# Kernel optimization log

Measured on AMD Instinct MI355X. Metric: run time of the kernel, lower is better.

The kernel has to match this reference:

```python
import jax, jax.numpy as jnp
import numpy as np

CH = (16, 32, 16)
T_STEPS = 30
THRESH = 1.0


def conv3d(x, w, b):
    # x: (B, Cin, D, H, W), w: (Cout, Cin, kD, kH, kW), stride 2, VALID
    y = jax.lax.conv_general_dilated(
        x, w, window_strides=(2, 2, 2), padding='VALID',
        dimension_numbers=('NCDHW', 'OIDHW', 'NCDHW'))
    return y + b[None, :, None, None, None]


def setup_inputs() -> dict:
    key = jax.random.key(0)
    ks = jax.random.split(key, 11)
    B = 4
    x = jax.random.normal(ks[0], (B, 24, 602, 602), jnp.float32)

    def uinit(k, shape, fan_in):
        bound = 1.0 / np.sqrt(fan_in)
        return jax.random.uniform(k, shape, jnp.float32, -bound, bound)

    fan1 = 1 * 3 * 15 * 15
    fan2 = CH[0] * 3 * 15 * 15
    fan3 = CH[1] * 3 * 15 * 15
    w1 = uinit(ks[1], (CH[0], 1, 3, 15, 15), fan1)
    b1 = uinit(ks[2], (CH[0],), fan1)
    w2 = uinit(ks[3], (CH[1], CH[0], 3, 15, 15), fan2)
    b2 = uinit(ks[4], (CH[1],), fan2)
    w3 = uinit(ks[5], (CH[2], CH[1], 3, 15, 15), fan3)
    b3 = uinit(ks[6], (CH[2],), fan3)
    F1 = 21632 * CH[2] // 16  # 21632 for CH[2]=16
    fc1_w = uinit(ks[7], (512, F1), F1)
    fc1_b = uinit(ks[8], (512,), F1)
    fc2_w = uinit(ks[9], (54, 512), 512)
    fc2_b = uinit(ks[10], (54,), 512)
    return dict(x=x, w1=w1, b1=b1, w2=w2, b2=b2, w3=w3, b3=b3,
                fc1_w=fc1_w, fc1_b=fc1_b, fc2_w=fc2_w, fc2_b=fc2_b)


def _forward(x, w1, b1, w2, b2, w3, b3, fc1_w, fc1_b, fc2_w, fc2_b):
    B = x.shape[0]
    # avg_pool2d(kernel=2): (B,24,602,602) -> (B,24,301,301)
    xp = x.reshape(B, 24, 301, 2, 301, 2).mean(axis=(3, 5))
    h = xp[:, None]  # (B,1,24,301,301)
    h = jax.nn.relu(conv3d(h, w1, b1))  # (B,16,11,144,144)
    h = jax.nn.relu(conv3d(h, w2, b2))  # (B,32,5,65,65)
    h = jax.nn.relu(conv3d(h, w3, b3))  # (B,16,2,26,26)
    x_snn = h.reshape(B, -1)            # (B, 21632)

    sgn = jnp.sign(x_snn)
    prob = jnp.abs(x_snn) * 0.5

    def step(carry, k):
        m0, m1 = carry
        r = jax.random.uniform(k, x_snn.shape, x_snn.dtype)
        # Poisson encoding with straight-through gradient to x_snn
        spikes = (prob > r).astype(x_snn.dtype) * sgn
        p_in = jax.lax.stop_gradient(spikes - x_snn) + x_snn
        m0 = m0 + p_in @ fc1_w.T + fc1_b
        # LIF: threshold, subtract, spike with surrogate (pass-through where fired)
        fire = m0 > THRESH
        ex = jnp.where(fire, m0, 0.0)
        m0 = m0 - ex
        out = jnp.where(fire, ex - jax.lax.stop_gradient(ex) + 1.0, 0.0)
        m1 = m1 + out @ fc2_w.T + fc2_b
        return (m0, m1), None

    keys = jax.random.split(jax.random.key(42), T_STEPS)
    init = (jnp.zeros((B, 512), x_snn.dtype), jnp.zeros((B, 54), x_snn.dtype))
    (_, m1), _ = jax.lax.scan(step, init, keys)
    return m1


def reference(x, w1, b1, w2, b2, w3, b3, fc1_w, fc1_b, fc2_w, fc2_b):
    return _forward(x, w1, b1, w2, b2, w3, b3, fc1_w, fc1_b, fc2_w, fc2_b)
```

## Files before the change

### kernel.cpp

```cpp
#include <hip/hip_runtime.h>
#include <stdint.h>

struct SnnKeys { unsigned int k0[30]; unsigned int k1[30]; };

__host__ __device__ static inline void tf2x32(unsigned int k0, unsigned int k1,
                                              unsigned int& x0, unsigned int& x1) {
  unsigned int ks2 = k0 ^ k1 ^ 0x1BD11BDAu;
#define TF_RND(r) { x0 += x1; x1 = (x1 << (r)) | (x1 >> (32 - (r))); x1 ^= x0; }
  x0 += k0; x1 += k1;
  TF_RND(13) TF_RND(15) TF_RND(26) TF_RND(6)
  x0 += k1; x1 += ks2 + 1u;
  TF_RND(17) TF_RND(29) TF_RND(16) TF_RND(24)
  x0 += ks2; x1 += k0 + 2u;
  TF_RND(13) TF_RND(15) TF_RND(26) TF_RND(6)
  x0 += k0; x1 += k1 + 3u;
  TF_RND(17) TF_RND(29) TF_RND(16) TF_RND(24)
  x0 += k1; x1 += ks2 + 4u;
  TF_RND(13) TF_RND(15) TF_RND(26) TF_RND(6)
  x0 += ks2; x1 += k0 + 5u;
#undef TF_RND
}

#define POOL_N (4 * 24 * 301 * 301)

__global__ __launch_bounds__(256) void k_pool(const float* __restrict__ x,
                                              float* __restrict__ xp) {
  int i = blockIdx.x * 256 + threadIdx.x;
  if (i >= POOL_N) return;
  int j = i % 301;
  int rest = i / 301;
  int r = rest % 301;
  int bc = rest / 301;
  const float* src = x + ((size_t)bc * 602 + 2 * r) * 602 + 2 * j;
  float2 a = *(const float2*)src;
  float2 b = *(const float2*)(src + 602);
  xp[i] = 0.25f * ((a.x + a.y) + (b.x + b.y));
}

__global__ __launch_bounds__(256) void k_wt2(const float* __restrict__ w2,
                                             float* __restrict__ w2t) {
  int i = blockIdx.x * 256 + threadIdx.x;
  if (i >= 345600) return;
  int co = i & 31;
  int rest = i >> 5;
  int ci = rest / 675;
  int k675 = rest - ci * 675;
  w2t[i] = w2[((size_t)co * 16 + ci) * 675 + k675];
}

__global__ __launch_bounds__(256) void k_wt3(const float* __restrict__ w3,
                                             float* __restrict__ w3t) {
  int i = blockIdx.x * 256 + threadIdx.x;
  if (i >= 345600) return;
  int co = i & 15;
  int rest = i >> 4;
  int ci = rest / 675;
  int k675 = rest - ci * 675;
  w3t[i] = w3[((size_t)co * 32 + ci) * 675 + k675];
}

__global__ __launch_bounds__(256) void k_conv1(const float* __restrict__ xp,
                                               const float* __restrict__ w1,
                                               const float* __restrict__ b1,
                                               float* __restrict__ h1) {
  __shared__ alignas(16) float in_e[25 * 152];
  __shared__ alignas(16) float in_o[25 * 152];
  const int tid = threadIdx.x;
  const int wave = __builtin_amdgcn_readfirstlane(tid >> 6);
  const int lane = tid & 63;
  const int cog = wave >> 1, sg = wave & 1;
  const int cob = cog * 8;
  const int bz = blockIdx.y;
  const int b = bz / 11, d = bz % 11;
  const int s0 = blockIdx.x * 512;
  const int y0 = s0 / 144;

  int sq[4], be[4];
  bool vq[4];
#pragma unroll
  for (int q = 0; q < 4; ++q) {
    int s = s0 + sg * 256 + q * 64 + lane;
    vq[q] = (s < 20736);
    int sc = vq[q] ? s : 20735;
    int y = sc / 144, xx = sc - y * 144;
    sq[q] = s;
    be[q] = 2 * (y - y0) * 152 + xx;
  }

  float acc[8][4] = {};

  for (int kd = 0; kd < 3; ++kd) {
    __syncthreads();
    const int din = 2 * d + kd;
    const float* src = xp + (size_t)(b * 24 + din) * 90601;
    for (int i = tid; i < 25 * 301; i += 256) {
      int r = i / 301, c = i - r * 301;
      int gr = 2 * y0 + r;
      float v = (gr < 301) ? src[gr * 301 + c] : 0.0f;
      ((c & 1) ? in_o : in_e)[r * 152 + (c >> 1)] = v;
    }
    __syncthreads();
    const float* wp = w1 + cob * 675 + kd * 225;
    for (int kh = 0; kh < 15; ++kh) {
      float e[4][8], o[4][7];
#pragma unroll
      for (int q = 0; q < 4; ++q) {
        const float* pe = in_e + be[q] + kh * 152;
        const float* po = in_o + be[q] + kh * 152;
#pragma unroll
        for (int j = 0; j < 8; ++j) e[q][j] = pe[j];
#pragma unroll
        for (int j = 0; j < 7; ++j) o[q][j] = po[j];
      }
      const float* wk = wp + kh * 15;
#pragma unroll
      for (int j = 0; j < 8; ++j) {
#pragma unroll
        for (int c = 0; c < 8; ++c) {
          float wv = wk[c * 675 + 2 * j];
#pragma unroll
          for (int q = 0; q < 4; ++q) acc[c][q] += wv * e[q][j];
        }
      }
#pragma unroll
      for (int j = 0; j < 7; ++j) {
#pragma unroll
        for (int c = 0; c < 8; ++c) {
          float wv = wk[c * 675 + 2 * j + 1];
#pragma unroll
          for (int q = 0; q < 4; ++q) acc[c][q] += wv * o[q][j];
        }
      }
    }
  }
#pragma unroll
  for (int q = 0; q < 4; ++q) {
    if (vq[q]) {
#pragma unroll
      for (int c = 0; c < 8; ++c) {
        float v = acc[c][q] + b1[cob + c];
        h1[((size_t)(b * 16 + cob + c) * 11 + d) * 20736 + sq[q]] = fmaxf(v, 0.0f);
      }
    }
  }
}

__global__ __launch_bounds__(256) void k_conv2(const float* __restrict__ h1,
                                               const float* __restrict__ w2t,
                                               float* __restrict__ h2p) {
  __shared__ alignas(16) float in_e[23 * 76];
  __shared__ alignas(16) float in_o[23 * 76];
  const int tid = threadIdx.x;
  const int wave = __builtin_amdgcn_readfirstlane(tid >> 6);
  const int lane = tid & 63;
  const int cob = wave * 8;
  const int bz = blockIdx.y;
  const int cig = bz & 1;
  const int t5 = bz >> 1;
  const int b = t5 / 5, d = t5 % 5;
  const int g0 = blockIdx.x * 64;
  const int r0 = g0 / 17;
  const int row0 = 2 * r0;

  const int gi = g0 + lane;
  const int r = gi / 17;
  const int g = gi - r * 17;
  const int lr = r - r0;
  const int x0 = g * 4;
  const bool valid = (gi < 1105);

  float acc[8][4] = {};

  for (int cil = 0; cil < 8; ++cil) {
    const int ci = cig * 8 + cil;
    for (int kd = 0; kd < 3; ++kd) {
      __syncthreads();
      const int din = 2 * d + kd;
      const float* src = h1 + (size_t)((b * 16 + ci) * 11 + din) * 20736;
      for (int i = tid; i < 23 * 36; i += 256) {
        int irr = i / 36, c4 = i - irr * 36;
        int gr = row0 + irr;
        float4 v = {0.0f, 0.0f, 0.0f, 0.0f};
        if (gr < 144) v = *(const float4*)(src + gr * 144 + c4 * 4);
        *(float2*)&in_e[irr * 76 + 2 * c4] = make_float2(v.x, v.z);
        *(float2*)&in_o[irr * 76 + 2 * c4] = make_float2(v.y, v.w);
      }
      __syncthreads();
      const float* wkb = w2t + (size_t)(ci * 3 + kd) * 225 * 32 + cob;
      const float* pe0 = in_e + (2 * lr) * 76 + x0;
      const float* po0 = in_o + (2 * lr) * 76 + x0;
#pragma unroll 5
      for (int kh = 0; kh < 15; ++kh) {
        float4 e0 = *(const float4*)(pe0 + kh * 76);
        float4 e1 = *(const float4*)(pe0 + kh * 76 + 4);
        float4 e2 = *(const float4*)(pe0 + kh * 76 + 8);
        float4 o0 = *(const float4*)(po0 + kh * 76);
        float4 o1 = *(const float4*)(po0 + kh * 76 + 4);
        float4 o2 = *(const float4*)(po0 + kh * 76 + 8);
        float E[12] = {e0.x, e0.y, e0.z, e0.w, e1.x, e1.y, e1.z, e1.w,
                       e2.x, e2.y, e2.z, e2.w};
        float O[12] = {o0.x, o0.y, o0.z, o0.w, o1.x, o1.y, o1.z, o1.w,
                       o2.x, o2.y, o2.z, o2.w};
        const float* wk = wkb + kh * 480;
#pragma unroll
        for (int m = 0; m < 8; ++m) {
#pragma unroll
          for (int c = 0; c < 8; ++c) {
            float wv = wk[m * 64 + c];
#pragma unroll
            for (int u = 0; u < 4; ++u) acc[c][u] += wv * E[m + u];
          }
        }
#pragma unroll
        for (int m = 0; m < 7; ++m) {
#pragma unroll
          for (int c = 0; c < 8; ++c) {
            float wv = wk[m * 64 + 32 + c];
#pragma unroll
            for (int u = 0; u < 4; ++u) acc[c][u] += wv * O[m + u];
          }
        }
      }
    }
  }
  if (valid) {
    float* dst = h2p + (size_t)cig * 2704000 +
                 ((size_t)(b * 32 + cob) * 5 + d) * 4225 + r * 65 + x0;
#pragma unroll
    for (int c = 0; c < 8; ++c) {
#pragma unroll
      for (int u = 0; u < 4; ++u) {
        if (x0 + u < 65) dst[(size_t)c * 5 * 4225 + u] = acc[c][u];
      }
    }
  }
}

__global__ __launch_bounds__(256) void k_h2fix(const float* __restrict__ p,
                                               const float* __restrict__ b2,
                                               float* __restrict__ h2) {
  int i = blockIdx.x * 256 + threadIdx.x;
  if (i >= 2704000) return;
  int co = (i / 21125) & 31;
  float v = p[i] + p[2704000 + i] + b2[co];
  h2[i] = fmaxf(v, 0.0f);
}

__global__ __launch_bounds__(256) void k_conv3(const float* __restrict__ h2,
                                               const float* __restrict__ w3t,
                                               float* __restrict__ h3p) {
  __shared__ alignas(16) float in_e[55 * 36];
  __shared__ alignas(16) float in_o[55 * 36];
  const int tid = threadIdx.x;
  const int wave = __builtin_amdgcn_readfirstlane(tid >> 6);
  const int lane = tid & 63;
  const int cog = wave >> 1, sg = wave & 1;
  const int cob = cog * 8;
  const int bz = blockIdx.y;
  const int b = bz >> 1, d = bz & 1;
  const int cig = blockIdx.z;
  const int s0 = blockIdx.x * 512;
  const int y0 = s0 / 26;

  int sq[4], be[4];
  bool vq[4];
#pragma unroll
  for (int q = 0; q < 4; ++q) {
    int s = s0 + sg * 256 + q * 64 + lane;
    vq[q] = (s < 676);
    int sc = vq[q] ? s : 675;
    int y = sc / 26, xx = sc - y * 26;
    sq[q] = s;
    be[q] = 2 * (y - y0) * 36 + xx;
  }

  float acc[8][4] = {};

  for (int cil = 0; cil < 2; ++cil) {
    const int ci = cig * 2 + cil;
    for (int kd = 0; kd < 3; ++kd) {
      __syncthreads();
      const int din = 2 * d + kd;
      const float* src = h2 + (size_t)((b * 32 + ci) * 5 + din) * 4225;
      for (int i = tid; i < 55 * 65; i += 256) {
        int r = i / 65, c = i - r * 65;
        int gr = 2 * y0 + r;
        float v = (gr < 65) ? src[gr * 65 + c] : 0.0f;
        ((c & 1) ? in_o : in_e)[r * 36 + (c >> 1)] = v;
      }
      __syncthreads();
      const float* wkbase = w3t + (size_t)(ci * 3 + kd) * 225 * 16 + cob;
      for (int kh = 0; kh < 15; ++kh) {
        float e[4][8], o[4][7];
#pragma unroll
        for (int q = 0; q < 4; ++q) {
          const float* pe = in_e + be[q] + kh * 36;
          const float* po = in_o + be[q] + kh * 36;
#pragma unroll
          for (int j = 0; j < 8; ++j) e[q][j] = pe[j];
#pragma unroll
          for (int j = 0; j < 7; ++j) o[q][j] = po[j];
        }
        const float* wr = wkbase + kh * 15 * 16;
#pragma unroll
        for (int j = 0; j < 8; ++j) {
#pragma unroll
          for (int c = 0; c < 8; ++c) {
            float wv = wr[(2 * j) * 16 + c];
#pragma unroll
            for (int q = 0; q < 4; ++q) acc[c][q] += wv * e[q][j];
          }
        }
#pragma unroll
        for (int j = 0; j < 7; ++j) {
#pragma unroll
          for (int c = 0; c < 8; ++c) {
            float wv = wr[(2 * j + 1) * 16 + c];
#pragma unroll
            for (int q = 0; q < 4; ++q) acc[c][q] += wv * o[q][j];
          }
        }
      }
    }
  }
#pragma unroll
  for (int q = 0; q < 4; ++q) {
    if (vq[q]) {
#pragma unroll
      for (int c = 0; c < 8; ++c) {
        h3p[(size_t)cig * 86528 +
            ((size_t)(b * 16 + cob + c) * 2 + d) * 676 + sq[q]] = acc[c][q];
      }
    }
  }
}

__global__ __launch_bounds__(256) void k_h3fix(const float* __restrict__ h3p,
                                               const float* __restrict__ b3,
                                               float* __restrict__ prob) {
  int p = blockIdx.x * 256 + threadIdx.x;
  if (p >= 86528) return;
  int co = (p % 21632) / 1352;
  float x = b3[co];
  for (int g = 0; g < 16; ++g) x += h3p[(size_t)g * 86528 + p];
  prob[p] = 0.5f * fmaxf(x, 0.0f);
}

__global__ __launch_bounds__(256) void k_spike(const float* __restrict__ prob,
                                               float* __restrict__ spk,
                                               SnnKeys keys) {
  int p = blockIdx.x * 256 + threadIdx.x;
  int t = blockIdx.y;
  float pr = prob[p];
  unsigned int x0 = 0u, x1 = (unsigned int)p;
  tf2x32(keys.k0[t], keys.k1[t], x0, x1);
  unsigned int bits = x0 ^ x1;
  float r = __uint_as_float((bits >> 9) | 0x3f800000u) - 1.0f;
  spk[(size_t)t * 86528 + p] = (pr > r) ? 1.0f : 0.0f;
}

__global__ __launch_bounds__(128) void k_fc1(const float* __restrict__ spk,
                                             const float* __restrict__ fc1w,
                                             float* __restrict__ incp) {
  __shared__ alignas(16) float slds[16][128];
  __shared__ alignas(16) float wlds[16][32];
  const int tx = threadIdx.x;
  const int ty = threadIdx.y;
  const int tid = ty * 8 + tx;
  const int nt = blockIdx.x;
  const int kc = blockIdx.y;
  const int k0base = kc * 1664;

  float acc[8][4];
#pragma unroll
  for (int mi = 0; mi < 8; ++mi)
#pragma unroll
    for (int ni = 0; ni < 4; ++ni) acc[mi][ni] = 0.0f;

  for (int kb = 0; kb < 1664; kb += 16) {
    const int k0 = k0base + kb;
    __syncthreads();
    {
      int m = tid;
      float4 v[4] = {{0,0,0,0},{0,0,0,0},{0,0,0,0},{0,0,0,0}};
      if (m < 120) {
        const float4* s = (const float4*)(spk + (size_t)m * 21632 + k0);
        v[0] = s[0]; v[1] = s[1]; v[2] = s[2]; v[3] = s[3];
      }
#pragma unroll
      for (int q = 0; q < 4; ++q) {
        slds[4 * q + 0][m] = v[q].x;
        slds[4 * q + 1][m] = v[q].y;
        slds[4 * q + 2][m] = v[q].z;
        slds[4 * q + 3][m] = v[q].w;
      }
    }
    for (int e = tid; e < 512; e += 128) {
      int n = e >> 4, kk = e & 15;
      wlds[kk][n] = fc1w[(size_t)(nt * 32 + n) * 21632 + k0 + kk];
    }
    __syncthreads();
#pragma unroll
    for (int kk = 0; kk < 16; ++kk) {
      const float4 wv = *(const float4*)&wlds[kk][tx * 4];
      const float4 s0 = *(const float4*)&slds[kk][ty * 8];
      const float4 s1 = *(const float4*)&slds[kk][ty * 8 + 4];
      float sv[8] = {s0.x, s0.y, s0.z, s0.w, s1.x, s1.y, s1.z, s1.w};
      float wz[4] = {wv.x, wv.y, wv.z, wv.w};
#pragma unroll
      for (int mi = 0; mi < 8; ++mi)
#pragma unroll
        for (int ni = 0; ni < 4; ++ni) acc[mi][ni] += sv[mi] * wz[ni];
    }
  }
#pragma unroll
  for (int mi = 0; mi < 8; ++mi) {
    int m = ty * 8 + mi;
    if (m < 120) {
      float4 o = {acc[mi][0], acc[mi][1], acc[mi][2], acc[mi][3]};
      *(float4*)&incp[((size_t)kc * 120 + m) * 512 + nt * 32 + tx * 4] = o;
    }
  }
}

__global__ __launch_bounds__(256) void k_scan(const float* __restrict__ incp,
                                              const float* __restrict__ fc1b,
                                              float* __restrict__ cnt) {
  int i = blockIdx.x * 256 + threadIdx.x;
  int b = i >> 9, n = i & 511;
  float bias = fc1b[n];
  float m0 = 0.0f, c = 0.0f;
  for (int t = 0; t < 30; ++t) {
    int m = t * 4 + b;
    float s = bias;
    for (int kc = 0; kc < 13; ++kc) s += incp[((size_t)kc * 120 + m) * 512 + n];
    m0 += s;
    if (m0 > 1.0f) { c += 1.0f; m0 = 0.0f; }
  }
  cnt[i] = c;
}

__global__ __launch_bounds__(256) void k_final(const float* __restrict__ cnt,
                                               const float* __restrict__ fc2w,
                                               const float* __restrict__ fc2b,
                                               float* __restrict__ out) {
  int o = threadIdx.x;
  if (o >= 216) return;
  int b = o / 54, oo = o - b * 54;
  const float* w = fc2w + (size_t)oo * 512;
  const float* c = cnt + (size_t)b * 512;
  float s = 0.0f;
  for (int n = 0; n < 512; ++n) s += c[n] * w[n];
  out[o] = s + 30.0f * fc2b[oo];
}

extern "C" void kernel_launch(void* const* d_in, const int* in_sizes, int n_in,
                              void* d_out, int out_size, void* d_ws, size_t ws_size,
                              hipStream_t stream) {
  (void)in_sizes; (void)n_in; (void)out_size; (void)ws_size;
  const float* x    = (const float*)d_in[0];
  const float* w1   = (const float*)d_in[1];
  const float* b1   = (const float*)d_in[2];
  const float* w2   = (const float*)d_in[3];
  const float* b2   = (const float*)d_in[4];
  const float* w3   = (const float*)d_in[5];
  const float* b3   = (const float*)d_in[6];
  const float* fc1w = (const float*)d_in[7];
  const float* fc1b = (const float*)d_in[8];
  const float* fc2w = (const float*)d_in[9];
  const float* fc2b = (const float*)d_in[10];
  float* out = (float*)d_out;
  float* ws  = (float*)d_ws;

  float* xp   = ws;
  float* h1   = ws + 8697696;
  float* w2t  = ws + 8112000;
  float* h2p  = ws;
  float* h2   = ws + 5408000;
  float* w3t  = ws;
  float* h3p  = ws + 8697696;
  float* prob = h3p + 16 * 86528;
  float* spk  = prob + 86528;
  float* incp = spk + 2595840;
  float* cnt  = incp + 13 * 61440;

  SnnKeys keys;
  for (int t = 0; t < 30; ++t) {
    unsigned int a = 0u, bb = (unsigned int)t;
    tf2x32(0u, 42u, a, bb);
    keys.k0[t] = a; keys.k1[t] = bb;
  }

  k_pool <<<(POOL_N + 255) / 256, 256, 0, stream>>>(x, xp);
  k_conv1<<<dim3(41, 44),    256, 0, stream>>>(xp, w1, b1, h1);
  k_wt2  <<<1350, 256, 0, stream>>>(w2, w2t);
  k_conv2<<<dim3(18, 40),    256, 0, stream>>>(h1, w2t, h2p);
  k_h2fix<<<(2704000 + 255) / 256, 256, 0, stream>>>(h2p, b2, h2);
  k_wt3  <<<1350, 256, 0, stream>>>(w3, w3t);
  k_conv3<<<dim3(2, 8, 16),  256, 0, stream>>>(h2, w3t, h3p);
  k_h3fix<<<338, 256, 0, stream>>>(h3p, b3, prob);
  k_spike<<<dim3(338, 30),   256, 0, stream>>>(prob, spk, keys);
  k_fc1  <<<dim3(16, 13), dim3(8, 16), 0, stream>>>(spk, fc1w, incp);
  k_scan <<<8, 256, 0, stream>>>(incp, fc1b, cnt);
  k_final<<<1, 256, 0, stream>>>(cnt, fc2w, fc2b, out);
}
```

Before: 1.769 ms.

## Register-block conv1 outputs, swizzle shared tiles, and prefetch conv2 input stages

conv1 now gives each thread 4 adjacent output columns instead of 4 strided pixels. This reuses a sliding window of float4 shared loads across kw and allows a vectorized float4 store. Both conv1 and conv2 use an XOR-swizzled shared-memory layout to avoid bank conflicts, and they prefetch the next kh row's registers during compute. conv2 also loads the next (ci,kd) stage from global into registers while computing the current one, which hides global latency at the cost of extra registers and possible occupancy loss.

```diff
diff --git a/kernel.cpp b/kernel.cpp
--- a/kernel.cpp
+++ b/kernel.cpp
@@ -63,8 +63,8 @@
                                                const float* __restrict__ w1,
                                                const float* __restrict__ b1,
                                                float* __restrict__ h1) {
-  __shared__ alignas(16) float in_e[25 * 152];
-  __shared__ alignas(16) float in_o[25 * 152];
+  __shared__ alignas(16) float in_e[23 * 160];
+  __shared__ alignas(16) float in_o[23 * 160];
   const int tid = threadIdx.x;
   const int wave = __builtin_amdgcn_readfirstlane(tid >> 6);
   const int lane = tid & 63;
@@ -72,20 +72,17 @@
   const int cob = cog * 8;
   const int bz = blockIdx.y;
   const int b = bz / 11, d = bz % 11;
-  const int s0 = blockIdx.x * 512;
-  const int y0 = s0 / 144;
-
-  int sq[4], be[4];
-  bool vq[4];
-#pragma unroll
-  for (int q = 0; q < 4; ++q) {
-    int s = s0 + sg * 256 + q * 64 + lane;
-    vq[q] = (s < 20736);
-    int sc = vq[q] ? s : 20735;
-    int y = sc / 144, xx = sc - y * 144;
-    sq[q] = s;
-    be[q] = 2 * (y - y0) * 152 + xx;
-  }
+  const int g0 = blockIdx.x * 128;
+  const int r0 = g0 / 36;
+  const int row0 = 2 * r0;
+
+  const int gi0 = g0 + sg * 64 + lane;
+  const bool valid = (gi0 < 5184);
+  const int gi = valid ? gi0 : 5183;
+  const int y = gi / 36;
+  const int g = gi - y * 36;
+  const int lr = y - r0;
+  const int x0 = g * 4;
 
   float acc[8][4] = {};
 
@@ -93,54 +90,83 @@
     __syncthreads();
     const int din = 2 * d + kd;
     const float* src = xp + (size_t)(b * 24 + din) * 90601;
-    for (int i = tid; i < 25 * 301; i += 256) {
-      int r = i / 301, c = i - r * 301;
-      int gr = 2 * y0 + r;
+    for (int i = tid; i < 23 * 301; i += 256) {
+      int irr = i / 301, c = i - irr * 301;
+      int gr = row0 + irr;
       float v = (gr < 301) ? src[gr * 301 + c] : 0.0f;
-      ((c & 1) ? in_o : in_e)[r * 152 + (c >> 1)] = v;
+      int rh = irr & 7;
+      int idx = c >> 1;
+      int off = irr * 160 + (((idx >> 2) ^ rh) << 2) + (idx & 3);
+      ((c & 1) ? in_o : in_e)[off] = v;
     }
     __syncthreads();
     const float* wp = w1 + cob * 675 + kd * 225;
+    const int rbase = 2 * lr;
+    float4 E4[3], O4[3];
+    {
+      const int rr = rbase;
+      const int rh = rr & 7;
+      const int ba = rr * 160;
+#pragma unroll
+      for (int k = 0; k < 3; ++k) {
+        int of = ba + (((g + k) ^ rh) << 2);
+        E4[k] = *(const float4*)&in_e[of];
+        O4[k] = *(const float4*)&in_o[of];
+      }
+    }
+#pragma unroll 5
     for (int kh = 0; kh < 15; ++kh) {
-      float e[4][8], o[4][7];
-#pragma unroll
-      for (int q = 0; q < 4; ++q) {
-        const float* pe = in_e + be[q] + kh * 152;
-        const float* po = in_o + be[q] + kh * 152;
-#pragma unroll
-        for (int j = 0; j < 8; ++j) e[q][j] = pe[j];
-#pragma unroll
-        for (int j = 0; j < 7; ++j) o[q][j] = po[j];
-      }
+      float4 nE[3], nO[3];
+      if (kh < 14) {
+        const int rr = rbase + kh + 1;
+        const int rh = rr & 7;
+        const int ba = rr * 160;
+#pragma unroll
+        for (int k = 0; k < 3; ++k) {
+          int of = ba + (((g + k) ^ rh) << 2);
+          nE[k] = *(const float4*)&in_e[of];
+          nO[k] = *(const float4*)&in_o[of];
+        }
+      }
+      float E[12] = {E4[0].x, E4[0].y, E4[0].z, E4[0].w,
+                     E4[1].x, E4[1].y, E4[1].z, E4[1].w,
+                     E4[2].x, E4[2].y, E4[2].z, E4[2].w};
+      float O[12] = {O4[0].x, O4[0].y, O4[0].z, O4[0].w,
+                     O4[1].x, O4[1].y, O4[1].z, O4[1].w,
+                     O4[2].x, O4[2].y, O4[2].z, O4[2].w};
       const float* wk = wp + kh * 15;
 #pragma unroll
-      for (int j = 0; j < 8; ++j) {
+      for (int m = 0; m < 8; ++m) {
 #pragma unroll
         for (int c = 0; c < 8; ++c) {
-          float wv = wk[c * 675 + 2 * j];
-#pragma unroll
-          for (int q = 0; q < 4; ++q) acc[c][q] += wv * e[q][j];
-        }
-      }
-#pragma unroll
-      for (int j = 0; j < 7; ++j) {
+          float wv = wk[c * 675 + 2 * m];
+#pragma unroll
+          for (int u = 0; u < 4; ++u) acc[c][u] += wv * E[m + u];
+        }
+      }
+#pragma unroll
+      for (int m = 0; m < 7; ++m) {
 #pragma unroll
         for (int c = 0; c < 8; ++c) {
-          float wv = wk[c * 675 + 2 * j + 1];
-#pragma unroll
-          for (int q = 0; q < 4; ++q) acc[c][q] += wv * o[q][j];
-        }
-      }
-    }
-  }
-#pragma unroll
-  for (int q = 0; q < 4; ++q) {
-    if (vq[q]) {
-#pragma unroll
-      for (int c = 0; c < 8; ++c) {
-        float v = acc[c][q] + b1[cob + c];
-        h1[((size_t)(b * 16 + cob + c) * 11 + d) * 20736 + sq[q]] = fmaxf(v, 0.0f);
-      }
+          float wv = wk[c * 675 + 2 * m + 1];
+#pragma unroll
+          for (int u = 0; u < 4; ++u) acc[c][u] += wv * O[m + u];
+        }
+      }
+      if (kh < 14) {
+#pragma unroll
+        for (int k = 0; k < 3; ++k) { E4[k] = nE[k]; O4[k] = nO[k]; }
+      }
+    }
+  }
+  if (valid) {
+    float* dst = h1 + ((size_t)(b * 16 + cob) * 11 + d) * 20736 + y * 144 + x0;
+#pragma unroll
+    for (int c = 0; c < 8; ++c) {
+      float bv = b1[cob + c];
+      float4 o = {fmaxf(acc[c][0] + bv, 0.0f), fmaxf(acc[c][1] + bv, 0.0f),
+                  fmaxf(acc[c][2] + bv, 0.0f), fmaxf(acc[c][3] + bv, 0.0f)};
+      *(float4*)(dst + (size_t)c * 11 * 20736) = o;
     }
   }
 }
@@ -148,8 +174,8 @@
 __global__ __launch_bounds__(256) void k_conv2(const float* __restrict__ h1,
                                                const float* __restrict__ w2t,
                                                float* __restrict__ h2p) {
-  __shared__ alignas(16) float in_e[23 * 76];
-  __shared__ alignas(16) float in_o[23 * 76];
+  __shared__ alignas(16) float in_e[23 * 96];
+  __shared__ alignas(16) float in_o[23 * 96];
   const int tid = threadIdx.x;
   const int wave = __builtin_amdgcn_readfirstlane(tid >> 6);
   const int lane = tid & 63;
@@ -162,64 +188,112 @@
   const int r0 = g0 / 17;
   const int row0 = 2 * r0;
 
-  const int gi = g0 + lane;
+  const int gi0 = g0 + lane;
+  const bool valid = (gi0 < 1105);
+  const int gi = valid ? gi0 : 1104;
   const int r = gi / 17;
   const int g = gi - r * 17;
   const int lr = r - r0;
   const int x0 = g * 4;
-  const bool valid = (gi < 1105);
 
   float acc[8][4] = {};
-
-  for (int cil = 0; cil < 8; ++cil) {
+  float4 pre[4];
+
+  auto issue = [&](int st) {
+    const int cil = st / 3, kd = st - cil * 3;
     const int ci = cig * 8 + cil;
-    for (int kd = 0; kd < 3; ++kd) {
-      __syncthreads();
-      const int din = 2 * d + kd;
-      const float* src = h1 + (size_t)((b * 16 + ci) * 11 + din) * 20736;
-      for (int i = tid; i < 23 * 36; i += 256) {
+    const int din = 2 * d + kd;
+    const float* src = h1 + (size_t)((b * 16 + ci) * 11 + din) * 20736;
+#pragma unroll
+    for (int ii = 0; ii < 4; ++ii) {
+      int i = tid + ii * 256;
+      float4 v = {0.0f, 0.0f, 0.0f, 0.0f};
+      if (i < 828) {
         int irr = i / 36, c4 = i - irr * 36;
         int gr = row0 + irr;
-        float4 v = {0.0f, 0.0f, 0.0f, 0.0f};
         if (gr < 144) v = *(const float4*)(src + gr * 144 + c4 * 4);
-        *(float2*)&in_e[irr * 76 + 2 * c4] = make_float2(v.x, v.z);
-        *(float2*)&in_o[irr * 76 + 2 * c4] = make_float2(v.y, v.w);
-      }
-      __syncthreads();
-      const float* wkb = w2t + (size_t)(ci * 3 + kd) * 225 * 32 + cob;
-      const float* pe0 = in_e + (2 * lr) * 76 + x0;
-      const float* po0 = in_o + (2 * lr) * 76 + x0;
+      }
+      pre[ii] = v;
+    }
+  };
+
+  issue(0);
+  for (int st = 0; st < 24; ++st) {
+    __syncthreads();
+#pragma unroll
+    for (int ii = 0; ii < 4; ++ii) {
+      int i = tid + ii * 256;
+      if (i < 828) {
+        int irr = i / 36, c4 = i - irr * 36;
+        int rh = irr & 7;
+        int off = irr * 96 + (((c4 >> 1) ^ rh) << 2) + ((c4 & 1) << 1);
+        float4 v = pre[ii];
+        *(float2*)&in_e[off] = make_float2(v.x, v.z);
+        *(float2*)&in_o[off] = make_float2(v.y, v.w);
+      }
+    }
+    __syncthreads();
+    if (st < 23) issue(st + 1);
+
+    const int cil = st / 3, kd = st - cil * 3;
+    const int ci = cig * 8 + cil;
+    const float* wkb = w2t + (size_t)(ci * 3 + kd) * 225 * 32 + cob;
+
+    const int rbase = 2 * lr;
+    float4 E4[3], O4[3];
+    {
+      const int rr = rbase;
+      const int rh = rr & 7;
+      const int ba = rr * 96;
+#pragma unroll
+      for (int k = 0; k < 3; ++k) {
+        int of = ba + (((g + k) ^ rh) << 2);
+        E4[k] = *(const float4*)&in_e[of];
+        O4[k] = *(const float4*)&in_o[of];
+      }
+    }
 #pragma unroll 5
-      for (int kh = 0; kh < 15; ++kh) {
-        float4 e0 = *(const float4*)(pe0 + kh * 76);
-        float4 e1 = *(const float4*)(pe0 + kh * 76 + 4);
-        float4 e2 = *(const float4*)(pe0 + kh * 76 + 8);
-        float4 o0 = *(const float4*)(po0 + kh * 76);
-        float4 o1 = *(const float4*)(po0 + kh * 76 + 4);
-        float4 o2 = *(const float4*)(po0 + kh * 76 + 8);
-        float E[12] = {e0.x, e0.y, e0.z, e0.w, e1.x, e1.y, e1.z, e1.w,
-                       e2.x, e2.y, e2.z, e2.w};
-        float O[12] = {o0.x, o0.y, o0.z, o0.w, o1.x, o1.y, o1.z, o1.w,
-                       o2.x, o2.y, o2.z, o2.w};
-        const float* wk = wkb + kh * 480;
-#pragma unroll
-        for (int m = 0; m < 8; ++m) {
-#pragma unroll
-          for (int c = 0; c < 8; ++c) {
-            float wv = wk[m * 64 + c];
-#pragma unroll
-            for (int u = 0; u < 4; ++u) acc[c][u] += wv * E[m + u];
-          }
-        }
-#pragma unroll
-        for (int m = 0; m < 7; ++m) {
-#pragma unroll
-          for (int c = 0; c < 8; ++c) {
-            float wv = wk[m * 64 + 32 + c];
-#pragma unroll
-            for (int u = 0; u < 4; ++u) acc[c][u] += wv * O[m + u];
-          }
-        }
+    for (int kh = 0; kh < 15; ++kh) {
+      float4 nE[3], nO[3];
+      if (kh < 14) {
+        const int rr = rbase + kh + 1;
+        const int rh = rr & 7;
+        const int ba = rr * 96;
+#pragma unroll
+        for (int k = 0; k < 3; ++k) {
+          int of = ba + (((g + k) ^ rh) << 2);
+          nE[k] = *(const float4*)&in_e[of];
+          nO[k] = *(const float4*)&in_o[of];
+        }
+      }
+      float E[12] = {E4[0].x, E4[0].y, E4[0].z, E4[0].w,
+                     E4[1].x, E4[1].y, E4[1].z, E4[1].w,
+                     E4[2].x, E4[2].y, E4[2].z, E4[2].w};
+      float O[12] = {O4[0].x, O4[0].y, O4[0].z, O4[0].w,
+                     O4[1].x, O4[1].y, O4[1].z, O4[1].w,
+                     O4[2].x, O4[2].y, O4[2].z, O4[2].w};
+      const float* wk = wkb + kh * 480;
+#pragma unroll
+      for (int m = 0; m < 8; ++m) {
+#pragma unroll
+        for (int c = 0; c < 8; ++c) {
+          float wv = wk[m * 64 + c];
+#pragma unroll
+          for (int u = 0; u < 4; ++u) acc[c][u] += wv * E[m + u];
+        }
+      }
+#pragma unroll
+      for (int m = 0; m < 7; ++m) {
+#pragma unroll
+        for (int c = 0; c < 8; ++c) {
+          float wv = wk[m * 64 + 32 + c];
+#pragma unroll
+          for (int u = 0; u < 4; ++u) acc[c][u] += wv * O[m + u];
+        }
+      }
+      if (kh < 14) {
+#pragma unroll
+        for (int k = 0; k < 3; ++k) { E4[k] = nE[k]; O4[k] = nO[k]; }
       }
     }
   }
@@ -230,7 +304,7 @@
     for (int c = 0; c < 8; ++c) {
 #pragma unroll
       for (int u = 0; u < 4; ++u) {
-        if (x0 + u < 65) dst[(size_t)c * 5 * 4225 + u] = acc[c][u];
+        if (x0 + u < 65) dst[(size_t)c * 21125 + u] = acc[c][u];
       }
     }
   }
```

Measured after the change: 4.054 ms. 2.29x slower.

## Register-tile conv1 with sliding windows and split conv2 reduction three ways

Applied to the files above, without the earlier changes.

conv1 now gives each thread four adjacent output columns. One set of vectorized LDS row loads is reused across the overlapping 15-tap window, and results go out as float4 stores, replacing per-output scalar shared-memory reads. conv2's input-channel×depth reduction is split into three partitions instead of two, so the grid has 50% more blocks. h2fix now sums three partial buffers. This cuts LDS traffic in conv1 and improves load balance across CUs in conv2, at the cost of an extra partial buffer read/write and a reshuffled workspace layout.

```diff
diff --git a/kernel.cpp b/kernel.cpp
--- a/kernel.cpp
+++ b/kernel.cpp
@@ -63,8 +63,8 @@
                                                const float* __restrict__ w1,
                                                const float* __restrict__ b1,
                                                float* __restrict__ h1) {
-  __shared__ alignas(16) float in_e[25 * 152];
-  __shared__ alignas(16) float in_o[25 * 152];
+  __shared__ alignas(16) float in_e[23 * 152];
+  __shared__ alignas(16) float in_o[23 * 152];
   const int tid = threadIdx.x;
   const int wave = __builtin_amdgcn_readfirstlane(tid >> 6);
   const int lane = tid & 63;
@@ -72,20 +72,17 @@
   const int cob = cog * 8;
   const int bz = blockIdx.y;
   const int b = bz / 11, d = bz % 11;
-  const int s0 = blockIdx.x * 512;
-  const int y0 = s0 / 144;
-
-  int sq[4], be[4];
-  bool vq[4];
-#pragma unroll
-  for (int q = 0; q < 4; ++q) {
-    int s = s0 + sg * 256 + q * 64 + lane;
-    vq[q] = (s < 20736);
-    int sc = vq[q] ? s : 20735;
-    int y = sc / 144, xx = sc - y * 144;
-    sq[q] = s;
-    be[q] = 2 * (y - y0) * 152 + xx;
-  }
+  const int g0 = blockIdx.x * 128;
+  const int r0 = g0 / 36;
+  const int row0 = 2 * r0;
+
+  const int gi0 = g0 + sg * 64 + lane;
+  const bool valid = (gi0 < 5184);
+  const int gi = valid ? gi0 : 5183;
+  const int y = gi / 36;
+  const int g = gi - y * 36;
+  const int lr = y - r0;
+  const int x0 = g * 4;
 
   float acc[8][4] = {};
 
@@ -93,54 +90,57 @@
     __syncthreads();
     const int din = 2 * d + kd;
     const float* src = xp + (size_t)(b * 24 + din) * 90601;
-    for (int i = tid; i < 25 * 301; i += 256) {
-      int r = i / 301, c = i - r * 301;
-      int gr = 2 * y0 + r;
+    for (int i = tid; i < 23 * 301; i += 256) {
+      int irr = i / 301, c = i - irr * 301;
+      int gr = row0 + irr;
       float v = (gr < 301) ? src[gr * 301 + c] : 0.0f;
-      ((c & 1) ? in_o : in_e)[r * 152 + (c >> 1)] = v;
+      ((c & 1) ? in_o : in_e)[irr * 152 + (c >> 1)] = v;
     }
     __syncthreads();
     const float* wp = w1 + cob * 675 + kd * 225;
+    const float* pe0 = in_e + 2 * lr * 152 + x0;
+    const float* po0 = in_o + 2 * lr * 152 + x0;
+#pragma unroll 5
     for (int kh = 0; kh < 15; ++kh) {
-      float e[4][8], o[4][7];
-#pragma unroll
-      for (int q = 0; q < 4; ++q) {
-        const float* pe = in_e + be[q] + kh * 152;
-        const float* po = in_o + be[q] + kh * 152;
-#pragma unroll
-        for (int j = 0; j < 8; ++j) e[q][j] = pe[j];
-#pragma unroll
-        for (int j = 0; j < 7; ++j) o[q][j] = po[j];
-      }
+      float4 e0 = *(const float4*)(pe0 + kh * 152);
+      float4 e1 = *(const float4*)(pe0 + kh * 152 + 4);
+      float4 e2 = *(const float4*)(pe0 + kh * 152 + 8);
+      float4 o0 = *(const float4*)(po0 + kh * 152);
+      float4 o1 = *(const float4*)(po0 + kh * 152 + 4);
+      float4 o2 = *(const float4*)(po0 + kh * 152 + 8);
+      float E[12] = {e0.x, e0.y, e0.z, e0.w, e1.x, e1.y, e1.z, e1.w,
+                     e2.x, e2.y, e2.z, e2.w};
+      float O[12] = {o0.x, o0.y, o0.z, o0.w, o1.x, o1.y, o1.z, o1.w,
+                     o2.x, o2.y, o2.z, o2.w};
       const float* wk = wp + kh * 15;
 #pragma unroll
-      for (int j = 0; j < 8; ++j) {
+      for (int m = 0; m < 8; ++m) {
 #pragma unroll
         for (int c = 0; c < 8; ++c) {
-          float wv = wk[c * 675 + 2 * j];
-#pragma unroll
-          for (int q = 0; q < 4; ++q) acc[c][q] += wv * e[q][j];
-        }
-      }
-#pragma unroll
-      for (int j = 0; j < 7; ++j) {
+          float wv = wk[c * 675 + 2 * m];
+#pragma unroll
+          for (int u = 0; u < 4; ++u) acc[c][u] += wv * E[m + u];
+        }
+      }
+#pragma unroll
+      for (int m = 0; m < 7; ++m) {
 #pragma unroll
         for (int c = 0; c < 8; ++c) {
-          float wv = wk[c * 675 + 2 * j + 1];
-#pragma unroll
-          for (int q = 0; q < 4; ++q) acc[c][q] += wv * o[q][j];
-        }
-      }
-    }
-  }
-#pragma unroll
-  for (int q = 0; q < 4; ++q) {
-    if (vq[q]) {
-#pragma unroll
-      for (int c = 0; c < 8; ++c) {
-        float v = acc[c][q] + b1[cob + c];
-        h1[((size_t)(b * 16 + cob + c) * 11 + d) * 20736 + sq[q]] = fmaxf(v, 0.0f);
-      }
+          float wv = wk[c * 675 + 2 * m + 1];
+#pragma unroll
+          for (int u = 0; u < 4; ++u) acc[c][u] += wv * O[m + u];
+        }
+      }
+    }
+  }
+  if (valid) {
+    float* dst = h1 + ((size_t)(b * 16 + cob) * 11 + d) * 20736 + y * 144 + x0;
+#pragma unroll
+    for (int c = 0; c < 8; ++c) {
+      float bv = b1[cob + c];
+      float4 o = {fmaxf(acc[c][0] + bv, 0.0f), fmaxf(acc[c][1] + bv, 0.0f),
+                  fmaxf(acc[c][2] + bv, 0.0f), fmaxf(acc[c][3] + bv, 0.0f)};
+      *(float4*)(dst + (size_t)c * 11 * 20736) = o;
     }
   }
 }
@@ -155,82 +155,83 @@
   const int lane = tid & 63;
   const int cob = wave * 8;
   const int bz = blockIdx.y;
-  const int cig = bz & 1;
-  const int t5 = bz >> 1;
+  const int cig3 = bz % 3;
+  const int t5 = bz / 3;
   const int b = t5 / 5, d = t5 % 5;
   const int g0 = blockIdx.x * 64;
   const int r0 = g0 / 17;
   const int row0 = 2 * r0;
 
-  const int gi = g0 + lane;
+  const int gi0 = g0 + lane;
+  const bool valid = (gi0 < 1105);
+  const int gi = valid ? gi0 : 1104;
   const int r = gi / 17;
   const int g = gi - r * 17;
   const int lr = r - r0;
   const int x0 = g * 4;
-  const bool valid = (gi < 1105);
 
   float acc[8][4] = {};
 
-  for (int cil = 0; cil < 8; ++cil) {
-    const int ci = cig * 8 + cil;
-    for (int kd = 0; kd < 3; ++kd) {
-      __syncthreads();
-      const int din = 2 * d + kd;
-      const float* src = h1 + (size_t)((b * 16 + ci) * 11 + din) * 20736;
-      for (int i = tid; i < 23 * 36; i += 256) {
-        int irr = i / 36, c4 = i - irr * 36;
-        int gr = row0 + irr;
-        float4 v = {0.0f, 0.0f, 0.0f, 0.0f};
-        if (gr < 144) v = *(const float4*)(src + gr * 144 + c4 * 4);
-        *(float2*)&in_e[irr * 76 + 2 * c4] = make_float2(v.x, v.z);
-        *(float2*)&in_o[irr * 76 + 2 * c4] = make_float2(v.y, v.w);
-      }
-      __syncthreads();
-      const float* wkb = w2t + (size_t)(ci * 3 + kd) * 225 * 32 + cob;
-      const float* pe0 = in_e + (2 * lr) * 76 + x0;
-      const float* po0 = in_o + (2 * lr) * 76 + x0;
+  for (int s = 0; s < 16; ++s) {
+    const int u = cig3 * 16 + s;
+    const int ci = u / 3;
+    const int kd = u - 3 * ci;
+    __syncthreads();
+    const int din = 2 * d + kd;
+    const float* src = h1 + (size_t)((b * 16 + ci) * 11 + din) * 20736;
+    for (int i = tid; i < 23 * 36; i += 256) {
+      int irr = i / 36, c4 = i - irr * 36;
+      int gr = row0 + irr;
+      float4 v = {0.0f, 0.0f, 0.0f, 0.0f};
+      if (gr < 144) v = *(const float4*)(src + gr * 144 + c4 * 4);
+      *(float2*)&in_e[irr * 76 + 2 * c4] = make_float2(v.x, v.z);
+      *(float2*)&in_o[irr * 76 + 2 * c4] = make_float2(v.y, v.w);
+    }
+    __syncthreads();
+    const float* wkb = w2t + (size_t)(ci * 3 + kd) * 225 * 32 + cob;
+    const float* pe0 = in_e + 2 * lr * 76 + x0;
+    const float* po0 = in_o + 2 * lr * 76 + x0;
 #pragma unroll 5
-      for (int kh = 0; kh < 15; ++kh) {
-        float4 e0 = *(const float4*)(pe0 + kh * 76);
-        float4 e1 = *(const float4*)(pe0 + kh * 76 + 4);
-        float4 e2 = *(const float4*)(pe0 + kh * 76 + 8);
-        float4 o0 = *(const float4*)(po0 + kh * 76);
-        float4 o1 = *(const float4*)(po0 + kh * 76 + 4);
-        float4 o2 = *(const float4*)(po0 + kh * 76 + 8);
-        float E[12] = {e0.x, e0.y, e0.z, e0.w, e1.x, e1.y, e1.z, e1.w,
-                       e2.x, e2.y, e2.z, e2.w};
-        float O[12] = {o0.x, o0.y, o0.z, o0.w, o1.x, o1.y, o1.z, o1.w,
-                       o2.x, o2.y, o2.z, o2.w};
-        const float* wk = wkb + kh * 480;
-#pragma unroll
-        for (int m = 0; m < 8; ++m) {
-#pragma unroll
-          for (int c = 0; c < 8; ++c) {
-            float wv = wk[m * 64 + c];
-#pragma unroll
-            for (int u = 0; u < 4; ++u) acc[c][u] += wv * E[m + u];
-          }
-        }
-#pragma unroll
-        for (int m = 0; m < 7; ++m) {
-#pragma unroll
-          for (int c = 0; c < 8; ++c) {
-            float wv = wk[m * 64 + 32 + c];
-#pragma unroll
-            for (int u = 0; u < 4; ++u) acc[c][u] += wv * O[m + u];
-          }
+    for (int kh = 0; kh < 15; ++kh) {
+      float4 e0 = *(const float4*)(pe0 + kh * 76);
+      float4 e1 = *(const float4*)(pe0 + kh * 76 + 4);
+      float4 e2 = *(const float4*)(pe0 + kh * 76 + 8);
+      float4 o0 = *(const float4*)(po0 + kh * 76);
+      float4 o1 = *(const float4*)(po0 + kh * 76 + 4);
+      float4 o2 = *(const float4*)(po0 + kh * 76 + 8);
+      float E[12] = {e0.x, e0.y, e0.z, e0.w, e1.x, e1.y, e1.z, e1.w,
+                     e2.x, e2.y, e2.z, e2.w};
+      float O[12] = {o0.x, o0.y, o0.z, o0.w, o1.x, o1.y, o1.z, o1.w,
+                     o2.x, o2.y, o2.z, o2.w};
+      const float* wk = wkb + kh * 480;
+#pragma unroll
+      for (int m = 0; m < 8; ++m) {
+#pragma unroll
+        for (int c = 0; c < 8; ++c) {
+          float wv = wk[m * 64 + c];
+#pragma unroll
+          for (int u2 = 0; u2 < 4; ++u2) acc[c][u2] += wv * E[m + u2];
+        }
+      }
+#pragma unroll
+      for (int m = 0; m < 7; ++m) {
+#pragma unroll
+        for (int c = 0; c < 8; ++c) {
+          float wv = wk[m * 64 + 32 + c];
+#pragma unroll
+          for (int u2 = 0; u2 < 4; ++u2) acc[c][u2] += wv * O[m + u2];
         }
       }
     }
   }
   if (valid) {
-    float* dst = h2p + (size_t)cig * 2704000 +
+    float* dst = h2p + (size_t)cig3 * 2704000 +
                  ((size_t)(b * 32 + cob) * 5 + d) * 4225 + r * 65 + x0;
 #pragma unroll
     for (int c = 0; c < 8; ++c) {
 #pragma unroll
       for (int u = 0; u < 4; ++u) {
-        if (x0 + u < 65) dst[(size_t)c * 5 * 4225 + u] = acc[c][u];
+        if (x0 + u < 65) dst[(size_t)c * 21125 + u] = acc[c][u];
       }
     }
   }
@@ -242,7 +243,7 @@
   int i = blockIdx.x * 256 + threadIdx.x;
   if (i >= 2704000) return;
   int co = (i / 21125) & 31;
-  float v = p[i] + p[2704000 + i] + b2[co];
+  float v = p[i] + p[2704000 + i] + p[5408000 + i] + b2[co];
   h2[i] = fmaxf(v, 0.0f);
 }
 
@@ -476,13 +477,13 @@
   float* h1   = ws + 8697696;
   float* w2t  = ws + 8112000;
   float* h2p  = ws;
-  float* h2   = ws + 5408000;
+  float* h2   = ws + 8697696;
   float* w3t  = ws;
-  float* h3p  = ws + 8697696;
-  float* prob = h3p + 16 * 86528;
-  float* spk  = prob + 86528;
-  float* incp = spk + 2595840;
-  float* cnt  = incp + 13 * 61440;
+  float* h3p  = ws + 11401696;
+  float* prob = ws + 12786144;
+  float* spk  = ws + 12872672;
+  float* incp = ws + 15468512;
+  float* cnt  = ws + 16267232;
 
   SnnKeys keys;
   for (int t = 0; t < 30; ++t) {
@@ -494,7 +495,7 @@
   k_pool <<<(POOL_N + 255) / 256, 256, 0, stream>>>(x, xp);
   k_conv1<<<dim3(41, 44),    256, 0, stream>>>(xp, w1, b1, h1);
   k_wt2  <<<1350, 256, 0, stream>>>(w2, w2t);
-  k_conv2<<<dim3(18, 40),    256, 0, stream>>>(h1, w2t, h2p);
+  k_conv2<<<dim3(18, 60),    256, 0, stream>>>(h1, w2t, h2p);
   k_h2fix<<<(2704000 + 255) / 256, 256, 0, stream>>>(h2p, b2, h2);
   k_wt3  <<<1350, 256, 0, stream>>>(w3, w3t);
   k_conv3<<<dim3(2, 8, 16),  256, 0, stream>>>(h2, w3t, h3p);
```

Result: slower. 2.052 ms (+16.0%).

## Increase split-K partitioning for conv2, conv3 and fc1 to raise block counts

Applied to the files above, without the earlier changes.

Conv2 now splits its 48 (ci,kd) reduction slices three ways instead of two, conv3 gives each input channel its own block (32 partials instead of 16), and fc1 splits K into 26 chunks instead of 13. The reduce kernels (h2fix, h3fix, scan) are widened to sum the extra partials, and the workspace layout is reassigned to fit the larger partial buffers. The aim is more blocks and better CU occupancy on the reduction-heavy convolutions and the FC layer. The cost is more partial-sum traffic and extra global reads in the fix-up kernels.

```diff
diff --git a/kernel.cpp b/kernel.cpp
--- a/kernel.cpp
+++ b/kernel.cpp
@@ -155,82 +155,83 @@
   const int lane = tid & 63;
   const int cob = wave * 8;
   const int bz = blockIdx.y;
-  const int cig = bz & 1;
-  const int t5 = bz >> 1;
+  const int cig3 = bz % 3;
+  const int t5 = bz / 3;
   const int b = t5 / 5, d = t5 % 5;
   const int g0 = blockIdx.x * 64;
   const int r0 = g0 / 17;
   const int row0 = 2 * r0;
 
-  const int gi = g0 + lane;
+  const int gi0 = g0 + lane;
+  const bool valid = (gi0 < 1105);
+  const int gi = valid ? gi0 : 1104;
   const int r = gi / 17;
   const int g = gi - r * 17;
   const int lr = r - r0;
   const int x0 = g * 4;
-  const bool valid = (gi < 1105);
 
   float acc[8][4] = {};
 
-  for (int cil = 0; cil < 8; ++cil) {
-    const int ci = cig * 8 + cil;
-    for (int kd = 0; kd < 3; ++kd) {
-      __syncthreads();
-      const int din = 2 * d + kd;
-      const float* src = h1 + (size_t)((b * 16 + ci) * 11 + din) * 20736;
-      for (int i = tid; i < 23 * 36; i += 256) {
-        int irr = i / 36, c4 = i - irr * 36;
-        int gr = row0 + irr;
-        float4 v = {0.0f, 0.0f, 0.0f, 0.0f};
-        if (gr < 144) v = *(const float4*)(src + gr * 144 + c4 * 4);
-        *(float2*)&in_e[irr * 76 + 2 * c4] = make_float2(v.x, v.z);
-        *(float2*)&in_o[irr * 76 + 2 * c4] = make_float2(v.y, v.w);
-      }
-      __syncthreads();
-      const float* wkb = w2t + (size_t)(ci * 3 + kd) * 225 * 32 + cob;
-      const float* pe0 = in_e + (2 * lr) * 76 + x0;
-      const float* po0 = in_o + (2 * lr) * 76 + x0;
+  for (int s = 0; s < 16; ++s) {
+    const int u = cig3 * 16 + s;
+    const int ci = u / 3;
+    const int kd = u - 3 * ci;
+    __syncthreads();
+    const int din = 2 * d + kd;
+    const float* src = h1 + (size_t)((b * 16 + ci) * 11 + din) * 20736;
+    for (int i = tid; i < 23 * 36; i += 256) {
+      int irr = i / 36, c4 = i - irr * 36;
+      int gr = row0 + irr;
+      float4 v = {0.0f, 0.0f, 0.0f, 0.0f};
+      if (gr < 144) v = *(const float4*)(src + gr * 144 + c4 * 4);
+      *(float2*)&in_e[irr * 76 + 2 * c4] = make_float2(v.x, v.z);
+      *(float2*)&in_o[irr * 76 + 2 * c4] = make_float2(v.y, v.w);
+    }
+    __syncthreads();
+    const float* wkb = w2t + (size_t)(ci * 3 + kd) * 225 * 32 + cob;
+    const float* pe0 = in_e + 2 * lr * 76 + x0;
+    const float* po0 = in_o + 2 * lr * 76 + x0;
 #pragma unroll 5
-      for (int kh = 0; kh < 15; ++kh) {
-        float4 e0 = *(const float4*)(pe0 + kh * 76);
-        float4 e1 = *(const float4*)(pe0 + kh * 76 + 4);
-        float4 e2 = *(const float4*)(pe0 + kh * 76 + 8);
-        float4 o0 = *(const float4*)(po0 + kh * 76);
-        float4 o1 = *(const float4*)(po0 + kh * 76 + 4);
-        float4 o2 = *(const float4*)(po0 + kh * 76 + 8);
-        float E[12] = {e0.x, e0.y, e0.z, e0.w, e1.x, e1.y, e1.z, e1.w,
-                       e2.x, e2.y, e2.z, e2.w};
-        float O[12] = {o0.x, o0.y, o0.z, o0.w, o1.x, o1.y, o1.z, o1.w,
-                       o2.x, o2.y, o2.z, o2.w};
-        const float* wk = wkb + kh * 480;
-#pragma unroll
-        for (int m = 0; m < 8; ++m) {
-#pragma unroll
-          for (int c = 0; c < 8; ++c) {
-            float wv = wk[m * 64 + c];
-#pragma unroll
-            for (int u = 0; u < 4; ++u) acc[c][u] += wv * E[m + u];
-          }
+    for (int kh = 0; kh < 15; ++kh) {
+      float4 e0 = *(const float4*)(pe0 + kh * 76);
+      float4 e1 = *(const float4*)(pe0 + kh * 76 + 4);
+      float4 e2 = *(const float4*)(pe0 + kh * 76 + 8);
+      float4 o0 = *(const float4*)(po0 + kh * 76);
+      float4 o1 = *(const float4*)(po0 + kh * 76 + 4);
+      float4 o2 = *(const float4*)(po0 + kh * 76 + 8);
+      float E[12] = {e0.x, e0.y, e0.z, e0.w, e1.x, e1.y, e1.z, e1.w,
+                     e2.x, e2.y, e2.z, e2.w};
+      float O[12] = {o0.x, o0.y, o0.z, o0.w, o1.x, o1.y, o1.z, o1.w,
+                     o2.x, o2.y, o2.z, o2.w};
+      const float* wk = wkb + kh * 480;
+#pragma unroll
+      for (int m = 0; m < 8; ++m) {
+#pragma unroll
+        for (int c = 0; c < 8; ++c) {
+          float wv = wk[m * 64 + c];
+#pragma unroll
+          for (int u2 = 0; u2 < 4; ++u2) acc[c][u2] += wv * E[m + u2];
         }
-#pragma unroll
-        for (int m = 0; m < 7; ++m) {
-#pragma unroll
-          for (int c = 0; c < 8; ++c) {
-            float wv = wk[m * 64 + 32 + c];
-#pragma unroll
-            for (int u = 0; u < 4; ++u) acc[c][u] += wv * O[m + u];
-          }
+      }
+#pragma unroll
+      for (int m = 0; m < 7; ++m) {
+#pragma unroll
+        for (int c = 0; c < 8; ++c) {
+          float wv = wk[m * 64 + 32 + c];
+#pragma unroll
+          for (int u2 = 0; u2 < 4; ++u2) acc[c][u2] += wv * O[m + u2];
         }
       }
     }
   }
   if (valid) {
-    float* dst = h2p + (size_t)cig * 2704000 +
+    float* dst = h2p + (size_t)cig3 * 2704000 +
                  ((size_t)(b * 32 + cob) * 5 + d) * 4225 + r * 65 + x0;
 #pragma unroll
     for (int c = 0; c < 8; ++c) {
 #pragma unroll
       for (int u = 0; u < 4; ++u) {
-        if (x0 + u < 65) dst[(size_t)c * 5 * 4225 + u] = acc[c][u];
+        if (x0 + u < 65) dst[(size_t)c * 21125 + u] = acc[c][u];
       }
     }
   }
@@ -242,7 +243,7 @@
   int i = blockIdx.x * 256 + threadIdx.x;
   if (i >= 2704000) return;
   int co = (i / 21125) & 31;
-  float v = p[i] + p[2704000 + i] + b2[co];
+  float v = p[i] + p[2704000 + i] + p[5408000 + i] + b2[co];
   h2[i] = fmaxf(v, 0.0f);
 }
 
@@ -258,7 +259,7 @@
   const int cob = cog * 8;
   const int bz = blockIdx.y;
   const int b = bz >> 1, d = bz & 1;
-  const int cig = blockIdx.z;
+  const int ci = blockIdx.z;
   const int s0 = blockIdx.x * 512;
   const int y0 = s0 / 26;
 
@@ -276,49 +277,46 @@
 
   float acc[8][4] = {};
 
-  for (int cil = 0; cil < 2; ++cil) {
-    const int ci = cig * 2 + cil;
-    for (int kd = 0; kd < 3; ++kd) {
-      __syncthreads();
-      const int din = 2 * d + kd;
-      const float* src = h2 + (size_t)((b * 32 + ci) * 5 + din) * 4225;
-      for (int i = tid; i < 55 * 65; i += 256) {
-        int r = i / 65, c = i - r * 65;
-        int gr = 2 * y0 + r;
-        float v = (gr < 65) ? src[gr * 65 + c] : 0.0f;
-        ((c & 1) ? in_o : in_e)[r * 36 + (c >> 1)] = v;
-      }
-      __syncthreads();
-      const float* wkbase = w3t + (size_t)(ci * 3 + kd) * 225 * 16 + cob;
-      for (int kh = 0; kh < 15; ++kh) {
-        float e[4][8], o[4][7];
-#pragma unroll
-        for (int q = 0; q < 4; ++q) {
-          const float* pe = in_e + be[q] + kh * 36;
-          const float* po = in_o + be[q] + kh * 36;
-#pragma unroll
-          for (int j = 0; j < 8; ++j) e[q][j] = pe[j];
-#pragma unroll
-          for (int j = 0; j < 7; ++j) o[q][j] = po[j];
+  for (int kd = 0; kd < 3; ++kd) {
+    __syncthreads();
+    const int din = 2 * d + kd;
+    const float* src = h2 + (size_t)((b * 32 + ci) * 5 + din) * 4225;
+    for (int i = tid; i < 55 * 65; i += 256) {
+      int r = i / 65, c = i - r * 65;
+      int gr = 2 * y0 + r;
+      float v = (gr < 65) ? src[gr * 65 + c] : 0.0f;
+      ((c & 1) ? in_o : in_e)[r * 36 + (c >> 1)] = v;
+    }
+    __syncthreads();
+    const float* wkbase = w3t + (size_t)(ci * 3 + kd) * 225 * 16 + cob;
+    for (int kh = 0; kh < 15; ++kh) {
+      float e[4][8], o[4][7];
+#pragma unroll
+      for (int q = 0; q < 4; ++q) {
+        const float* pe = in_e + be[q] + kh * 36;
+        const float* po = in_o + be[q] + kh * 36;
+#pragma unroll
+        for (int j = 0; j < 8; ++j) e[q][j] = pe[j];
+#pragma unroll
+        for (int j = 0; j < 7; ++j) o[q][j] = po[j];
+      }
+      const float* wr = wkbase + kh * 15 * 16;
+#pragma unroll
+      for (int j = 0; j < 8; ++j) {
+#pragma unroll
+        for (int c = 0; c < 8; ++c) {
+          float wv = wr[(2 * j) * 16 + c];
+#pragma unroll
+          for (int q = 0; q < 4; ++q) acc[c][q] += wv * e[q][j];
         }
-        const float* wr = wkbase + kh * 15 * 16;
-#pragma unroll
-        for (int j = 0; j < 8; ++j) {
-#pragma unroll
-          for (int c = 0; c < 8; ++c) {
-            float wv = wr[(2 * j) * 16 + c];
-#pragma unroll
-            for (int q = 0; q < 4; ++q) acc[c][q] += wv * e[q][j];
-          }
-        }
-#pragma unroll
-        for (int j = 0; j < 7; ++j) {
-#pragma unroll
-          for (int c = 0; c < 8; ++c) {
-            float wv = wr[(2 * j + 1) * 16 + c];
-#pragma unroll
-            for (int q = 0; q < 4; ++q) acc[c][q] += wv * o[q][j];
-          }
+      }
+#pragma unroll
+      for (int j = 0; j < 7; ++j) {
+#pragma unroll
+        for (int c = 0; c < 8; ++c) {
+          float wv = wr[(2 * j + 1) * 16 + c];
+#pragma unroll
+          for (int q = 0; q < 4; ++q) acc[c][q] += wv * o[q][j];
         }
       }
     }
@@ -328,7 +326,7 @@
     if (vq[q]) {
 #pragma unroll
       for (int c = 0; c < 8; ++c) {
-        h3p[(size_t)cig * 86528 +
+        h3p[(size_t)ci * 86528 +
             ((size_t)(b * 16 + cob + c) * 2 + d) * 676 + sq[q]] = acc[c][q];
       }
     }
@@ -342,7 +340,7 @@
   if (p >= 86528) return;
   int co = (p % 21632) / 1352;
   float x = b3[co];
-  for (int g = 0; g < 16; ++g) x += h3p[(size_t)g * 86528 + p];
+  for (int g = 0; g < 32; ++g) x += h3p[(size_t)g * 86528 + p];
   prob[p] = 0.5f * fmaxf(x, 0.0f);
 }
 
@@ -369,7 +367,7 @@
   const int tid = ty * 8 + tx;
   const int nt = blockIdx.x;
   const int kc = blockIdx.y;
-  const int k0base = kc * 1664;
+  const int k0base = kc * 832;
 
   float acc[8][4];
 #pragma unroll
@@ -377,7 +375,7 @@
 #pragma unroll
     for (int ni = 0; ni < 4; ++ni) acc[mi][ni] = 0.0f;
 
-  for (int kb = 0; kb < 1664; kb += 16) {
+  for (int kb = 0; kb < 832; kb += 16) {
     const int k0 = k0base + kb;
     __syncthreads();
     {
@@ -433,7 +431,7 @@
   for (int t = 0; t < 30; ++t) {
     int m = t * 4 + b;
     float s = bias;
-    for (int kc = 0; kc < 13; ++kc) s += incp[((size_t)kc * 120 + m) * 512 + n];
+    for (int kc = 0; kc < 26; ++kc) s += incp[((size_t)kc * 120 + m) * 512 + n];
     m0 += s;
     if (m0 > 1.0f) { c += 1.0f; m0 = 0.0f; }
   }
@@ -476,13 +474,13 @@
   float* h1   = ws + 8697696;
   float* w2t  = ws + 8112000;
   float* h2p  = ws;
-  float* h2   = ws + 5408000;
+  float* h2   = ws + 8697696;
   float* w3t  = ws;
-  float* h3p  = ws + 8697696;
-  float* prob = h3p + 16 * 86528;
-  float* spk  = prob + 86528;
-  float* incp = spk + 2595840;
-  float* cnt  = incp + 13 * 61440;
+  float* h3p  = ws + 11401696;
+  float* prob = ws + 14170592;
+  float* spk  = ws + 14257120;
+  float* incp = ws + 16852960;
+  float* cnt  = ws + 18450400;
 
   SnnKeys keys;
   for (int t = 0; t < 30; ++t) {
@@ -494,13 +492,13 @@
   k_pool <<<(POOL_N + 255) / 256, 256, 0, stream>>>(x, xp);
   k_conv1<<<dim3(41, 44),    256, 0, stream>>>(xp, w1, b1, h1);
   k_wt2  <<<1350, 256, 0, stream>>>(w2, w2t);
-  k_conv2<<<dim3(18, 40),    256, 0, stream>>>(h1, w2t, h2p);
+  k_conv2<<<dim3(18, 60),    256, 0, stream>>>(h1, w2t, h2p);
   k_h2fix<<<(2704000 + 255) / 256, 256, 0, stream>>>(h2p, b2, h2);
   k_wt3  <<<1350, 256, 0, stream>>>(w3, w3t);
-  k_conv3<<<dim3(2, 8, 16),  256, 0, stream>>>(h2, w3t, h3p);
+  k_conv3<<<dim3(2, 8, 32),  256, 0, stream>>>(h2, w3t, h3p);
   k_h3fix<<<338, 256, 0, stream>>>(h3p, b3, prob);
   k_spike<<<dim3(338, 30),   256, 0, stream>>>(prob, spk, keys);
-  k_fc1  <<<dim3(16, 13), dim3(8, 16), 0, stream>>>(spk, fc1w, incp);
+  k_fc1  <<<dim3(16, 26), dim3(8, 16), 0, stream>>>(spk, fc1w, incp);
   k_scan <<<8, 256, 0, stream>>>(incp, fc1b, cnt);
   k_final<<<1, 256, 0, stream>>>(cnt, fc2w, fc2b, out);
 }
```

After: 1.562 ms. 1.13x faster.
